# Kernel tuning notes

Measured on AMD Instinct MI355X. Metric: run time of the kernel, lower is better.

Reference implementation:

```python
import jax, jax.numpy as jnp
import numpy as np

N_NODES = 100000  # total nodes (60k type-a + 40k type-b)
N_EDGES = 3200000


def spmm(rows, cols, vals, x):
    # y[r] = sum_e vals[e] * x[cols[e]] for edges with rows[e] == r  (COO SpMM)
    return jax.ops.segment_sum(vals[:, None] * x[cols], rows, num_segments=N_NODES)


def setup_inputs() -> dict:
    key = jax.random.key(0)
    ks = jax.random.split(key, 12)
    d_a, d_b, n_hid, n_out = 256, 128, 256, 64
    s = lambda d: (1.0 / np.sqrt(d)).astype(np.float32)
    return {
        "x_a": jax.random.normal(ks[0], (60000, d_a), dtype=jnp.float32),
        "x_b": jax.random.normal(ks[1], (40000, d_b), dtype=jnp.float32),
        "rows": jax.random.randint(ks[2], (N_EDGES,), 0, N_NODES, dtype=jnp.int32),
        "cols": jax.random.randint(ks[3], (N_EDGES,), 0, N_NODES, dtype=jnp.int32),
        "vals": jax.random.uniform(ks[4], (N_EDGES,), dtype=jnp.float32),
        "W1a": jax.random.normal(ks[5], (d_a, n_hid), dtype=jnp.float32) * s(d_a),
        "b1a": jnp.zeros((n_hid,), dtype=jnp.float32),
        "W1b": jax.random.normal(ks[6], (d_b, n_hid), dtype=jnp.float32) * s(d_b),
        "b1b": jnp.zeros((n_hid,), dtype=jnp.float32),
        "Wf": jax.random.normal(ks[7], (n_hid, n_hid), dtype=jnp.float32) * s(n_hid),
        "bf": jnp.zeros((n_hid,), dtype=jnp.float32),
        "W2": jax.random.normal(ks[8], (n_hid, n_out), dtype=jnp.float32) * s(n_hid),
        "b2": jnp.zeros((n_out,), dtype=jnp.float32),
    }


def reference(x_a, x_b, rows, cols, vals, W1a, b1a, W1b, b1b, Wf, bf, W2, b2):
    # per-type Linear + ReLU (dropout p=0 -> identity in eval/reference)
    h_a = jax.nn.relu(x_a @ W1a + b1a)  # [60000, n_hid]
    h_b = jax.nn.relu(x_b @ W1b + b1b)  # [40000, n_hid]
    x = jnp.concatenate([h_a, h_b], axis=0)  # [N_NODES, n_hid]
    # hop - 1 = 1 intermediate hop: Linear -> SpMM -> ReLU
    x = x @ Wf + bf
    x = spmm(rows, cols, vals, x)
    x = jax.nn.relu(x)
    # output projection then final SpMM aggregation
    x = x @ W2 + b2
    x = spmm(rows, cols, vals, x)  # [N_NODES, n_out]
    return x
```

## Files before the change

kernel.cpp:

```cpp
#include <hip/hip_runtime.h>

#define NN 100000
#define NE 3200000
#define NA 60000
#define NB 40000
#define NHID 256
#define NOUT 64

#define RPB 64
#define NBUCK 1563
#define PBLK 256
#define CHUNK 12500

#define WT_BLKS 704
#define G1_BLKS 938
#define G2_BLKS 626
#define G3_BLKS 1564

typedef unsigned short u16;
typedef unsigned int u32;
typedef __attribute__((ext_vector_type(8))) short short8;
typedef __attribute__((ext_vector_type(4))) float f32x4;

__device__ __forceinline__ float bf2f(u16 u) {
  return __uint_as_float(((u32)u) << 16);
}
__device__ __forceinline__ u16 f2bf(float f) {
  u32 u = __float_as_uint(f);
  u32 r = (u + 0x7fffu + ((u >> 16) & 1u)) >> 16;
  return (u16)r;
}
__device__ __forceinline__ float i8f(u32 dw, int b) {
  return (float)((int)(dw << (24 - 8 * b)) >> 24);
}

__device__ __forceinline__ void gload_lds16(const void* gsrc, void* ldst) {
  __builtin_amdgcn_global_load_lds(
      (const __attribute__((address_space(1))) void*)gsrc,
      (__attribute__((address_space(3))) void*)ldst, 16, 0, 0);
}

template <int BN, int RELU_OUT, int QUANT>
__device__ __forceinline__ void gemm_body(
    int bx, int by, const u16* __restrict__ A, const u16* __restrict__ Bt,
    const float* __restrict__ bias, void* __restrict__ Cout,
    float* __restrict__ scales, int M, int N, int K, u16* As, u16* Bs) {
  constexpr int FI = (BN == 128) ? 4 : 2;
  constexpr int WROWS = FI * 16;

  const int tid = threadIdx.x;
  const int w = tid >> 6;
  const int lane = tid & 63;
  const int bm = bx * 128;
  const int bn = by * BN;
  const int wr = (BN == 128) ? (w >> 1) : w;
  const int wc = (BN == 128) ? (w & 1) : 0;

  f32x4 acc[FI][4];
#pragma unroll
  for (int i = 0; i < FI; ++i)
#pragma unroll
    for (int j = 0; j < 4; ++j) acc[i][j] = (f32x4)0.f;

  for (int k0 = 0; k0 < K; k0 += 32) {
#pragma unroll
    for (int s = 0; s < 2; ++s) {
      const int inst = w * 2 + s;
      const int row = inst * 16 + (lane >> 2);
      int rg = bm + row;
      if (rg > M - 1) rg = M - 1;
      const int c = (lane & 3) ^ ((row >> 1) & 3);
      gload_lds16(A + (size_t)rg * K + k0 + c * 8, &As[inst * 512]);
    }
    if (BN == 128) {
#pragma unroll
      for (int s = 0; s < 2; ++s) {
        const int inst = w * 2 + s;
        const int row = inst * 16 + (lane >> 2);
        const int c = (lane & 3) ^ ((row >> 1) & 3);
        gload_lds16(Bt + (size_t)(bn + row) * K + k0 + c * 8,
                    &Bs[inst * 512]);
      }
    } else {
      const int inst = w;
      const int row = inst * 16 + (lane >> 2);
      const int c = (lane & 3) ^ ((row >> 1) & 3);
      gload_lds16(Bt + (size_t)(bn + row) * K + k0 + c * 8, &Bs[inst * 512]);
    }
    __syncthreads();

    const int kc = lane >> 4;
    short8 af[FI], bfr[4];
#pragma unroll
    for (int i = 0; i < FI; ++i) {
      const int row = wr * WROWS + i * 16 + (lane & 15);
      const int ch = kc ^ ((row >> 1) & 3);
      af[i] = *reinterpret_cast<const short8*>(&As[row * 32 + ch * 8]);
    }
#pragma unroll
    for (int j = 0; j < 4; ++j) {
      const int row = wc * 64 + j * 16 + (lane & 15);
      const int ch = kc ^ ((row >> 1) & 3);
      bfr[j] = *reinterpret_cast<const short8*>(&Bs[row * 32 + ch * 8]);
    }
#pragma unroll
    for (int i = 0; i < FI; ++i)
#pragma unroll
      for (int j = 0; j < 4; ++j)
        acc[i][j] = __builtin_amdgcn_mfma_f32_16x16x32_bf16(af[i], bfr[j],
                                                            acc[i][j], 0, 0, 0);
    __syncthreads();
  }

  if constexpr (QUANT == 1) {
    float bv[4];
#pragma unroll
    for (int j = 0; j < 4; ++j)
      bv[j] = bias[bn + wc * 64 + j * 16 + (lane & 15)];
    const int g = (bn >> 6) + wc;
    u32* zq = (u32*)Cout;
#pragma unroll
    for (int i = 0; i < FI; ++i) {
#pragma unroll
      for (int r = 0; r < 4; ++r) {
        float o[4];
#pragma unroll
        for (int j = 0; j < 4; ++j) o[j] = acc[i][j][r] + bv[j];
        float am = fmaxf(fmaxf(fabsf(o[0]), fabsf(o[1])),
                         fmaxf(fabsf(o[2]), fabsf(o[3])));
#pragma unroll
        for (int mk = 1; mk < 16; mk <<= 1) am = fmaxf(am, __shfl_xor(am, mk));
        const float sinv = am > 0.f ? 127.f / am : 0.f;
        const float scv = am > 0.f ? am / 127.f : 0.f;
        const int q0 = __float2int_rn(o[0] * sinv);
        const int q1 = __float2int_rn(o[1] * sinv);
        const int q2 = __float2int_rn(o[2] * sinv);
        const int q3 = __float2int_rn(o[3] * sinv);
        const u32 dw = (q0 & 0xff) | ((q1 & 0xff) << 8) | ((q2 & 0xff) << 16) |
                       ((q3 & 0xff) << 24);
        const int row = bm + wr * WROWS + i * 16 + (lane >> 4) * 4 + r;
        if (row < M) {
          zq[(size_t)row * 64 + g * 16 + (lane & 15)] = dw;
          if ((lane & 15) == 0) scales[(size_t)row * 4 + g] = scv;
        }
      }
    }
  } else if constexpr (QUANT == 2) {
    float bv[4];
#pragma unroll
    for (int j = 0; j < 4; ++j) bv[j] = bias[j * 16 + (lane & 15)];
    u32* zq = (u32*)Cout;
#pragma unroll
    for (int i = 0; i < FI; ++i) {
#pragma unroll
      for (int r = 0; r < 4; ++r) {
        float o[4];
#pragma unroll
        for (int j = 0; j < 4; ++j) o[j] = acc[i][j][r] + bv[j];
        float am = fmaxf(fmaxf(fabsf(o[0]), fabsf(o[1])),
                         fmaxf(fabsf(o[2]), fabsf(o[3])));
#pragma unroll
        for (int mk = 1; mk < 16; mk <<= 1) am = fmaxf(am, __shfl_xor(am, mk));
        const float sinv = am > 0.f ? 127.f / am : 0.f;
        const float scv = am > 0.f ? am / 127.f : 0.f;
        const int q0 = __float2int_rn(o[0] * sinv);
        const int q1 = __float2int_rn(o[1] * sinv);
        const int q2 = __float2int_rn(o[2] * sinv);
        const int q3 = __float2int_rn(o[3] * sinv);
        const u32 dw = (q0 & 0xff) | ((q1 & 0xff) << 8) | ((q2 & 0xff) << 16) |
                       ((q3 & 0xff) << 24);
        const int row = bm + wr * WROWS + i * 16 + (lane >> 4) * 4 + r;
        if (row < M) {
          zq[(size_t)row * 16 + (lane & 15)] = dw;
          if ((lane & 15) == 0) scales[row] = scv;
        }
      }
    }
  } else {
    u16* C = (u16*)Cout;
#pragma unroll
    for (int i = 0; i < FI; ++i) {
#pragma unroll
      for (int j = 0; j < 4; ++j) {
        const int col = bn + wc * 64 + j * 16 + (lane & 15);
        const float bv = bias[col];
#pragma unroll
        for (int r = 0; r < 4; ++r) {
          const int row = bm + wr * WROWS + i * 16 + (lane >> 4) * 4 + r;
          if (row < M) {
            float o = acc[i][j][r] + bv;
            if (RELU_OUT) o = fmaxf(o, 0.f);
            C[(size_t)row * N + col] = f2bf(o);
          }
        }
      }
    }
  }
}

__device__ __forceinline__ void gemm_af32(
    int bx, int by, const float* __restrict__ Af, const u16* __restrict__ Bt,
    const float* __restrict__ bias, u16* __restrict__ C, int M, int K,
    u16* As, u16* Bs) {
  constexpr int N = 256;
  const int tid = threadIdx.x;
  const int w = tid >> 6;
  const int lane = tid & 63;
  const int bm = bx * 128;
  const int bn = by * 128;
  const int wr = w >> 1;
  const int wc = w & 1;

  f32x4 acc[4][4];
#pragma unroll
  for (int i = 0; i < 4; ++i)
#pragma unroll
    for (int j = 0; j < 4; ++j) acc[i][j] = (f32x4)0.f;

  const int arow = tid >> 1;
  const int ahalf = tid & 1;
  int arg = bm + arow;
  if (arg > M - 1) arg = M - 1;
  const int asw = (arow >> 1) & 3;

  for (int k0 = 0; k0 < K; k0 += 32) {
#pragma unroll
    for (int s = 0; s < 2; ++s) {
      const int inst = w * 2 + s;
      const int row = inst * 16 + (lane >> 2);
      const int c = (lane & 3) ^ ((row >> 1) & 3);
      gload_lds16(Bt + (size_t)(bn + row) * K + k0 + c * 8, &Bs[inst * 512]);
    }
    {
      const float4* src = reinterpret_cast<const float4*>(
          Af + (size_t)arg * K + k0 + ahalf * 16);
      const float4 v0 = src[0], v1 = src[1], v2 = src[2], v3 = src[3];
      short8 lo, hi;
      lo[0] = (short)f2bf(v0.x); lo[1] = (short)f2bf(v0.y);
      lo[2] = (short)f2bf(v0.z); lo[3] = (short)f2bf(v0.w);
      lo[4] = (short)f2bf(v1.x); lo[5] = (short)f2bf(v1.y);
      lo[6] = (short)f2bf(v1.z); lo[7] = (short)f2bf(v1.w);
      hi[0] = (short)f2bf(v2.x); hi[1] = (short)f2bf(v2.y);
      hi[2] = (short)f2bf(v2.z); hi[3] = (short)f2bf(v2.w);
      hi[4] = (short)f2bf(v3.x); hi[5] = (short)f2bf(v3.y);
      hi[6] = (short)f2bf(v3.z); hi[7] = (short)f2bf(v3.w);
      short8* dst = reinterpret_cast<short8*>(As + arow * 32);
      dst[(ahalf * 2) ^ asw] = lo;
      dst[(ahalf * 2 + 1) ^ asw] = hi;
    }
    __syncthreads();

    const int kc = lane >> 4;
    short8 af[4], bfr[4];
#pragma unroll
    for (int i = 0; i < 4; ++i) {
      const int row = wr * 64 + i * 16 + (lane & 15);
      const int ch = kc ^ ((row >> 1) & 3);
      af[i] = *reinterpret_cast<const short8*>(&As[row * 32 + ch * 8]);
    }
#pragma unroll
    for (int j = 0; j < 4; ++j) {
      const int row = wc * 64 + j * 16 + (lane & 15);
      const int ch = kc ^ ((row >> 1) & 3);
      bfr[j] = *reinterpret_cast<const short8*>(&Bs[row * 32 + ch * 8]);
    }
#pragma unroll
    for (int i = 0; i < 4; ++i)
#pragma unroll
      for (int j = 0; j < 4; ++j)
        acc[i][j] = __builtin_amdgcn_mfma_f32_16x16x32_bf16(af[i], bfr[j],
                                                            acc[i][j], 0, 0, 0);
    __syncthreads();
  }

#pragma unroll
  for (int i = 0; i < 4; ++i) {
#pragma unroll
    for (int j = 0; j < 4; ++j) {
      const int col = bn + wc * 64 + j * 16 + (lane & 15);
      const float bv = bias[col];
#pragma unroll
      for (int r = 0; r < 4; ++r) {
        const int row = bm + wr * 64 + i * 16 + (lane >> 4) * 4 + r;
        if (row < M) {
          float o = fmaxf(acc[i][j][r] + bv, 0.f);
          C[(size_t)row * N + col] = f2bf(o);
        }
      }
    }
  }
}

template <int BN, int RELU_OUT, int QUANT>
__global__ __launch_bounds__(256) void gemm_mfma(
    const u16* __restrict__ A, const u16* __restrict__ Bt,
    const float* __restrict__ bias, void* __restrict__ Cout,
    float* __restrict__ scales, int M, int N, int K) {
  __shared__ __align__(16) u16 As[128 * 32];
  __shared__ __align__(16) u16 Bs[BN * 32];
  gemm_body<BN, RELU_OUT, QUANT>(blockIdx.x, blockIdx.y, A, Bt, bias, Cout,
                                 scales, M, N, K, As, Bs);
}

__global__ __launch_bounds__(256) void prep(
    const float* __restrict__ W1a, const float* __restrict__ W1b,
    const float* __restrict__ Wf, const float* __restrict__ W2,
    u16* __restrict__ W1at, u16* __restrict__ W1bt, u16* __restrict__ Wft,
    u16* __restrict__ W2t, const int* __restrict__ rows,
    int* __restrict__ cnt) {
  __shared__ int hsh[NBUCK];
  const int b = blockIdx.x;
  const int tid = threadIdx.x;
  if (b < WT_BLKS) {
    const int i = b * 256 + tid;
    if (i < 65536) {
      const int n = i >> 8, k = i & 255;
      W1at[i] = f2bf(W1a[k * 256 + n]);
    } else if (i < 98304) {
      const int t = i - 65536;
      const int n = t >> 7, k = t & 127;
      W1bt[t] = f2bf(W1b[k * 256 + n]);
    } else if (i < 163840) {
      const int t = i - 98304;
      const int n = t >> 8, k = t & 255;
      Wft[t] = f2bf(Wf[k * 256 + n]);
    } else if (i < 180224) {
      const int t = i - 163840;
      const int n = t >> 8, p = t & 255;
      const int f = ((p >> 6) << 6) + ((p & 3) << 4) + ((p >> 2) & 15);
      W2t[t] = f2bf(W2[f * 64 + n]);
    }
  } else {
    const int blk = b - WT_BLKS;
    for (int i = tid; i < NBUCK; i += 256) hsh[i] = 0;
    __syncthreads();
    const int s = blk * CHUNK;
    const int e = s + CHUNK;
    for (int i = s + tid; i < e; i += 256) atomicAdd(&hsh[rows[i] >> 6], 1);
    __syncthreads();
    for (int i = tid; i < NBUCK; i += 256) cnt[i * PBLK + blk] = hsh[i];
  }
}

__global__ __launch_bounds__(256) void gemm12_s1(
    const float* __restrict__ xa, const u16* __restrict__ W1at,
    const float* __restrict__ b1a, const float* __restrict__ xb,
    const u16* __restrict__ W1bt, const float* __restrict__ b1b,
    u16* __restrict__ h, int* __restrict__ cnt, int* __restrict__ btot) {
  __shared__ __align__(16) u16 As[128 * 32];
  __shared__ __align__(16) u16 Bs[128 * 32];
  const int b = blockIdx.x;
  if (b < G1_BLKS) {
    gemm_af32(b % 469, b / 469, xa, W1at, b1a, h, NA, 256, As, Bs);
  } else if (b < G1_BLKS + G2_BLKS) {
    const int t = b - G1_BLKS;
    gemm_af32(t % 313, t / 313, xb, W1bt, b1b, h + (size_t)NA * NHID, NB, 128,
              As, Bs);
  } else {
    int* lds = (int*)As;
    const int bu = b - (G1_BLKS + G2_BLKS);
    const int t = threadIdx.x;
    const int v = cnt[bu * PBLK + t];
    lds[t] = v;
    __syncthreads();
#pragma unroll
    for (int off = 1; off < 256; off <<= 1) {
      const int x = (t >= off) ? lds[t - off] : 0;
      __syncthreads();
      lds[t] += x;
      __syncthreads();
    }
    cnt[bu * PBLK + t] = lds[t] - v;
    if (t == 255) btot[bu] = lds[255];
  }
}

__global__ __launch_bounds__(256) void gemm3_s2_p3(
    const u16* __restrict__ h, const u16* __restrict__ Wft,
    const float* __restrict__ bfv, u32* __restrict__ zq,
    float* __restrict__ zscale, const int* __restrict__ btot,
    int* __restrict__ bstart, const int* __restrict__ rows,
    const int* __restrict__ cols, const float* __restrict__ vals,
    const int* __restrict__ cnt, int2* __restrict__ edges) {
  __shared__ __align__(16) u16 As[128 * 32];
  __shared__ __align__(16) u16 Bs[128 * 32];
  const int b = blockIdx.x;
  const int t = threadIdx.x;
  if (b < G3_BLKS) {
    gemm_body<128, 0, 1>(b % 782, b / 782, h, Wft, bfv, zq, zscale, NN, NHID,
                         256, As, Bs);
  } else if (b == G3_BLKS) {
    int* lds = (int*)As;
    int carry = 0;
    for (int base = 0; base < NBUCK; base += 256) {
      const int i = base + t;
      const int v = (i < NBUCK) ? btot[i] : 0;
      lds[t] = v;
      __syncthreads();
#pragma unroll
      for (int off = 1; off < 256; off <<= 1) {
        const int x = (t >= off) ? lds[t - off] : 0;
        __syncthreads();
        lds[t] += x;
        __syncthreads();
      }
      const int excl = lds[t] - v;
      const int tot = lds[255];
      if (i < NBUCK) bstart[i] = carry + excl;
      __syncthreads();
      carry += tot;
    }
    if (t == 0) bstart[NBUCK] = NE;
  } else {
    const int blk = b - (G3_BLKS + 1);
    int* lbs = (int*)As;
    int* tmp = (int*)Bs;
    int carry = 0;
    for (int base = 0; base < NBUCK; base += 256) {
      const int i = base + t;
      const int v = (i < NBUCK) ? btot[i] : 0;
      tmp[t] = v;
      __syncthreads();
#pragma unroll
      for (int off = 1; off < 256; off <<= 1) {
        const int x = (t >= off) ? tmp[t - off] : 0;
        __syncthreads();
        tmp[t] += x;
        __syncthreads();
      }
      if (i < NBUCK) lbs[i] = carry + tmp[t] - v;
      const int tot = tmp[255];
      __syncthreads();
      carry += tot;
    }
    for (int bu = t; bu < NBUCK; bu += 256) lbs[bu] += cnt[bu * PBLK + blk];
    __syncthreads();
    const int s = blk * CHUNK;
    const int e = s + CHUNK;
    for (int i = s + t; i < e; i += 256) {
      const int r = rows[i];
      const int pos = atomicAdd(&lbs[r >> 6], 1);
      edges[pos] = make_int2(cols[i] | ((r & 63) << 17), __float_as_int(vals[i]));
    }
  }
}

__global__ __launch_bounds__(256) void sort_bucket(
    const int* __restrict__ bstart, const int2* __restrict__ edges,
    int2* __restrict__ edges2, int* __restrict__ rptr) {
  __shared__ int hist[RPB];
  __shared__ int sc[RPB];
  __shared__ int cur[RPB];
  const int bu = blockIdx.x;
  const int t = threadIdx.x;
  const int s = bstart[bu], e = bstart[bu + 1];
  if (t < RPB) hist[t] = 0;
  __syncthreads();
  for (int i = s + t; i < e; i += 256)
    atomicAdd(&hist[(edges[i].x >> 17) & 63], 1);
  __syncthreads();
  const int hv = (t < RPB) ? hist[t] : 0;
  if (t < RPB) sc[t] = hv;
  __syncthreads();
#pragma unroll
  for (int off = 1; off < RPB; off <<= 1) {
    const int x = (t >= off && t < RPB) ? sc[t - off] : 0;
    __syncthreads();
    if (t < RPB) sc[t] += x;
    __syncthreads();
  }
  if (t < RPB) {
    const int base = s + sc[t] - hv;
    cur[t] = base;
    const int grow = bu * RPB + t;
    if (grow < NN) rptr[grow] = base;
  }
  if (bu == 0 && t == 0) rptr[NN] = NE;
  __syncthreads();
  for (int i = s + t; i < e; i += 256) {
    const int2 ed = edges[i];
    const int lr = (ed.x >> 17) & 63;
    const int pos = atomicAdd(&cur[lr], 1);
    edges2[pos] = make_int2(ed.x & 0x1FFFF, ed.y);
  }
}

__global__ __launch_bounds__(256) void spmm256_q8(
    const int* __restrict__ ptr, const int2* __restrict__ edges,
    const u32* __restrict__ Zq, const float* __restrict__ scales,
    u16* __restrict__ Yb) {
  const int wid = (int)((blockIdx.x * (size_t)256 + threadIdx.x) >> 6);
  const int lane = threadIdx.x & 63;
  if (wid >= NN) return;
  const int s = ptr[wid], e = ptr[wid + 1];
  const int gsel = lane >> 4;
  float a0 = 0.f, a1 = 0.f, a2 = 0.f, a3 = 0.f;
  int j = s;
  for (; j + 7 < e; j += 8) {
    int2 ed[8];
#pragma unroll
    for (int q = 0; q < 8; ++q) ed[q] = edges[j + q];
    u32 dw[8];
    float sc[8];
#pragma unroll
    for (int q = 0; q < 8; ++q) {
      dw[q] = Zq[(size_t)ed[q].x * 64 + lane];
      sc[q] = scales[(size_t)ed[q].x * 4 + gsel];
    }
#pragma unroll
    for (int q = 0; q < 8; ++q) {
      const float vs = __int_as_float(ed[q].y) * sc[q];
      a0 += vs * i8f(dw[q], 0);
      a1 += vs * i8f(dw[q], 1);
      a2 += vs * i8f(dw[q], 2);
      a3 += vs * i8f(dw[q], 3);
    }
  }
  for (; j < e; ++j) {
    const int2 e0 = edges[j];
    const u32 dw = Zq[(size_t)e0.x * 64 + lane];
    const float vs =
        __int_as_float(e0.y) * scales[(size_t)e0.x * 4 + gsel];
    a0 += vs * i8f(dw, 0);
    a1 += vs * i8f(dw, 1);
    a2 += vs * i8f(dw, 2);
    a3 += vs * i8f(dw, 3);
  }
  ushort4 o;
  o.x = f2bf(fmaxf(a0, 0.f));
  o.y = f2bf(fmaxf(a1, 0.f));
  o.z = f2bf(fmaxf(a2, 0.f));
  o.w = f2bf(fmaxf(a3, 0.f));
  reinterpret_cast<ushort4*>(Yb + (size_t)wid * 256)[lane] = o;
}

__global__ __launch_bounds__(256) void spmm64_q8(
    const int* __restrict__ ptr, const int2* __restrict__ edges,
    const u32* __restrict__ Z2q, const float* __restrict__ zsc2,
    float* __restrict__ Y) {
  const int wid = (int)((blockIdx.x * (size_t)256 + threadIdx.x) >> 6);
  const int lane = threadIdx.x & 63;
  if (wid >= NN) return;
  const int s = ptr[wid], e = ptr[wid + 1];
  const int dwi = lane & 15;
  const int byi = lane >> 4;
  float acc = 0.f;
  int j = s;
  for (; j + 7 < e; j += 8) {
    int2 ed[8];
#pragma unroll
    for (int q = 0; q < 8; ++q) ed[q] = edges[j + q];
    u32 dw[8];
    float sc[8];
#pragma unroll
    for (int q = 0; q < 8; ++q) {
      dw[q] = Z2q[(size_t)ed[q].x * 16 + dwi];
      sc[q] = zsc2[ed[q].x];
    }
#pragma unroll
    for (int q = 0; q < 8; ++q)
      acc += __int_as_float(ed[q].y) * sc[q] * i8f(dw[q], byi);
  }
  for (; j < e; ++j) {
    const int2 e0 = edges[j];
    const u32 dw = Z2q[(size_t)e0.x * 16 + dwi];
    acc += __int_as_float(e0.y) * zsc2[e0.x] * i8f(dw, byi);
  }
  Y[(size_t)wid * 64 + lane] = acc;
}

extern "C" void kernel_launch(void* const* d_in, const int* in_sizes, int n_in,
                              void* d_out, int out_size, void* d_ws,
                              size_t ws_size, hipStream_t stream) {
  const float* x_a  = (const float*)d_in[0];
  const float* x_b  = (const float*)d_in[1];
  const int*   rows = (const int*)d_in[2];
  const int*   cols = (const int*)d_in[3];
  const float* vals = (const float*)d_in[4];
  const float* W1a  = (const float*)d_in[5];
  const float* b1a  = (const float*)d_in[6];
  const float* W1b  = (const float*)d_in[7];
  const float* b1b  = (const float*)d_in[8];
  const float* Wf   = (const float*)d_in[9];
  const float* bf   = (const float*)d_in[10];
  const float* W2   = (const float*)d_in[11];
  const float* b2   = (const float*)d_in[12];
  float* out = (float*)d_out;

  char* p = (char*)d_ws;
  u16* h    = (u16*)p;  p += (size_t)NN * NHID * 2;
  u32* zq   = (u32*)p;  p += (size_t)NN * 64 * 4;
  float* zscale = (float*)p; p += (size_t)NN * 4 * 4;
  u32* z2q  = (u32*)p;  p += (size_t)NN * 16 * 4;
  float* zsc2 = (float*)p; p += (size_t)NN * 4;
  int2* edges2 = (int2*)p; p += (size_t)NE * 8;
  u16* W1at = (u16*)p;  p += 256 * 256 * 2;
  u16* W1bt = (u16*)p;  p += 256 * 128 * 2;
  u16* Wft  = (u16*)p;  p += 256 * 256 * 2;
  u16* W2t  = (u16*)p;  p += 64 * 256 * 2;
  int2* edges = (int2*)p; p += (size_t)NE * 8;
  int* cnt    = (int*)p;  p += (size_t)NBUCK * PBLK * 4;
  int* btot   = (int*)p;  p += (size_t)((NBUCK + 3) & ~3) * 4;
  int* bstart = (int*)p;  p += (size_t)((NBUCK + 4) & ~3) * 4;
  int* rptr   = (int*)p;  p += (size_t)(NN + 4) * 4;
  u16* s1b = h;

  prep<<<WT_BLKS + PBLK, 256, 0, stream>>>(W1a, W1b, Wf, W2, W1at, W1bt, Wft,
                                           W2t, rows, cnt);

  gemm12_s1<<<G1_BLKS + G2_BLKS + NBUCK, 256, 0, stream>>>(
      x_a, W1at, b1a, x_b, W1bt, b1b, h, cnt, btot);

  gemm3_s2_p3<<<G3_BLKS + 1 + PBLK, 256, 0, stream>>>(
      h, Wft, bf, zq, zscale, btot, bstart, rows, cols, vals, cnt, edges);

  sort_bucket<<<NBUCK, 256, 0, stream>>>(bstart, edges, edges2, rptr);

  spmm256_q8<<<(NN * 64 + 255) / 256, 256, 0, stream>>>(rptr, edges2, zq,
                                                        zscale, s1b);
  gemm_mfma<64, 0, 2><<<dim3((NN + 127) / 128, 1), 256, 0, stream>>>(
      s1b, W2t, b2, z2q, zsc2, NN, NOUT, 256);
  spmm64_q8<<<(NN * 64 + 255) / 256, 256, 0, stream>>>(rptr, edges2, z2q,
                                                       zsc2, out);
}
```

Baseline: 479.4 us.

## Pack sorted edges into 32-bit words and widen GEMM blocks to full N

Sorted CSR edges are packed into one 32-bit word each, holding a 17-bit column index and the edge value as fp16 in the upper 15 bits (sign bit dropped, which is fine because the values are non-negative). This halves the edge traffic in both SpMM passes. The first-layer and Wf GEMMs now run with 512-thread blocks that each cover all 256 output columns, so the A tile is loaded once instead of twice and the block count halves. The cost is reduced precision on the edge values and larger per-block LDS, and the scan kernels are adapted to the new block size.

```diff
diff --git a/kernel.cpp b/kernel.cpp
--- a/kernel.cpp
+++ b/kernel.cpp
@@ -13,9 +13,9 @@
 #define CHUNK 12500
 
 #define WT_BLKS 704
-#define G1_BLKS 938
-#define G2_BLKS 626
-#define G3_BLKS 1564
+#define G1_BLKS 469
+#define G2_BLKS 313
+#define G3_BLKS 782
 
 typedef unsigned short u16;
 typedef unsigned int u32;
@@ -33,6 +33,18 @@
 __device__ __forceinline__ float i8f(u32 dw, int b) {
   return (float)((int)(dw << (24 - 8 * b)) >> 24);
 }
+__device__ __forceinline__ u16 f2h(float f) {
+  _Float16 h = (_Float16)f;
+  u16 r;
+  __builtin_memcpy(&r, &h, 2);
+  return r;
+}
+__device__ __forceinline__ float h2f(u32 b15) {
+  u16 hb = (u16)b15;
+  _Float16 h;
+  __builtin_memcpy(&h, &hb, 2);
+  return (float)h;
+}
 
 __device__ __forceinline__ void gload_lds16(const void* gsrc, void* ldst) {
   __builtin_amdgcn_global_load_lds(
@@ -40,60 +52,46 @@
       (__attribute__((address_space(3))) void*)ldst, 16, 0, 0);
 }
 
-template <int BN, int RELU_OUT, int QUANT>
-__device__ __forceinline__ void gemm_body(
-    int bx, int by, const u16* __restrict__ A, const u16* __restrict__ Bt,
+template <int QUANT>
+__device__ __forceinline__ void gemm8_body(
+    int bx, const u16* __restrict__ A, const u16* __restrict__ Bt,
     const float* __restrict__ bias, void* __restrict__ Cout,
-    float* __restrict__ scales, int M, int N, int K, u16* As, u16* Bs) {
-  constexpr int FI = (BN == 128) ? 4 : 2;
-  constexpr int WROWS = FI * 16;
-
+    float* __restrict__ scales, int M, int K, u16* As, u16* Bs) {
   const int tid = threadIdx.x;
   const int w = tid >> 6;
   const int lane = tid & 63;
   const int bm = bx * 128;
-  const int bn = by * BN;
-  const int wr = (BN == 128) ? (w >> 1) : w;
-  const int wc = (BN == 128) ? (w & 1) : 0;
-
-  f32x4 acc[FI][4];
-#pragma unroll
-  for (int i = 0; i < FI; ++i)
+  const int wr = w >> 2;
+  const int wc = w & 3;
+
+  f32x4 acc[4][4];
+#pragma unroll
+  for (int i = 0; i < 4; ++i)
 #pragma unroll
     for (int j = 0; j < 4; ++j) acc[i][j] = (f32x4)0.f;
 
   for (int k0 = 0; k0 < K; k0 += 32) {
+    {
+      const int row = w * 16 + (lane >> 2);
+      int rg = bm + row;
+      if (rg > M - 1) rg = M - 1;
+      const int c = (lane & 3) ^ ((row >> 1) & 3);
+      gload_lds16(A + (size_t)rg * K + k0 + c * 8, &As[w * 512]);
+    }
 #pragma unroll
     for (int s = 0; s < 2; ++s) {
       const int inst = w * 2 + s;
       const int row = inst * 16 + (lane >> 2);
-      int rg = bm + row;
-      if (rg > M - 1) rg = M - 1;
       const int c = (lane & 3) ^ ((row >> 1) & 3);
-      gload_lds16(A + (size_t)rg * K + k0 + c * 8, &As[inst * 512]);
-    }
-    if (BN == 128) {
-#pragma unroll
-      for (int s = 0; s < 2; ++s) {
-        const int inst = w * 2 + s;
-        const int row = inst * 16 + (lane >> 2);
-        const int c = (lane & 3) ^ ((row >> 1) & 3);
-        gload_lds16(Bt + (size_t)(bn + row) * K + k0 + c * 8,
-                    &Bs[inst * 512]);
-      }
-    } else {
-      const int inst = w;
-      const int row = inst * 16 + (lane >> 2);
-      const int c = (lane & 3) ^ ((row >> 1) & 3);
-      gload_lds16(Bt + (size_t)(bn + row) * K + k0 + c * 8, &Bs[inst * 512]);
+      gload_lds16(Bt + (size_t)row * K + k0 + c * 8, &Bs[inst * 512]);
     }
     __syncthreads();
 
     const int kc = lane >> 4;
-    short8 af[FI], bfr[4];
-#pragma unroll
-    for (int i = 0; i < FI; ++i) {
-      const int row = wr * WROWS + i * 16 + (lane & 15);
+    short8 af[4], bfr[4];
+#pragma unroll
+    for (int i = 0; i < 4; ++i) {
+      const int row = wr * 64 + i * 16 + (lane & 15);
       const int ch = kc ^ ((row >> 1) & 3);
       af[i] = *reinterpret_cast<const short8*>(&As[row * 32 + ch * 8]);
     }
@@ -104,7 +102,7 @@
       bfr[j] = *reinterpret_cast<const short8*>(&Bs[row * 32 + ch * 8]);
     }
 #pragma unroll
-    for (int i = 0; i < FI; ++i)
+    for (int i = 0; i < 4; ++i)
 #pragma unroll
       for (int j = 0; j < 4; ++j)
         acc[i][j] = __builtin_amdgcn_mfma_f32_16x16x32_bf16(af[i], bfr[j],
@@ -115,12 +113,11 @@
   if constexpr (QUANT == 1) {
     float bv[4];
 #pragma unroll
-    for (int j = 0; j < 4; ++j)
-      bv[j] = bias[bn + wc * 64 + j * 16 + (lane & 15)];
-    const int g = (bn >> 6) + wc;
+    for (int j = 0; j < 4; ++j) bv[j] = bias[wc * 64 + j * 16 + (lane & 15)];
+    const int g = wc;
     u32* zq = (u32*)Cout;
 #pragma unroll
-    for (int i = 0; i < FI; ++i) {
+    for (int i = 0; i < 4; ++i) {
 #pragma unroll
       for (int r = 0; r < 4; ++r) {
         float o[4];
@@ -138,59 +135,27 @@
         const int q3 = __float2int_rn(o[3] * sinv);
         const u32 dw = (q0 & 0xff) | ((q1 & 0xff) << 8) | ((q2 & 0xff) << 16) |
                        ((q3 & 0xff) << 24);
-        const int row = bm + wr * WROWS + i * 16 + (lane >> 4) * 4 + r;
+        const int row = bm + wr * 64 + i * 16 + (lane >> 4) * 4 + r;
         if (row < M) {
           zq[(size_t)row * 64 + g * 16 + (lane & 15)] = dw;
           if ((lane & 15) == 0) scales[(size_t)row * 4 + g] = scv;
         }
       }
     }
-  } else if constexpr (QUANT == 2) {
-    float bv[4];
-#pragma unroll
-    for (int j = 0; j < 4; ++j) bv[j] = bias[j * 16 + (lane & 15)];
-    u32* zq = (u32*)Cout;
-#pragma unroll
-    for (int i = 0; i < FI; ++i) {
-#pragma unroll
-      for (int r = 0; r < 4; ++r) {
-        float o[4];
-#pragma unroll
-        for (int j = 0; j < 4; ++j) o[j] = acc[i][j][r] + bv[j];
-        float am = fmaxf(fmaxf(fabsf(o[0]), fabsf(o[1])),
-                         fmaxf(fabsf(o[2]), fabsf(o[3])));
-#pragma unroll
-        for (int mk = 1; mk < 16; mk <<= 1) am = fmaxf(am, __shfl_xor(am, mk));
-        const float sinv = am > 0.f ? 127.f / am : 0.f;
-        const float scv = am > 0.f ? am / 127.f : 0.f;
-        const int q0 = __float2int_rn(o[0] * sinv);
-        const int q1 = __float2int_rn(o[1] * sinv);
-        const int q2 = __float2int_rn(o[2] * sinv);
-        const int q3 = __float2int_rn(o[3] * sinv);
-        const u32 dw = (q0 & 0xff) | ((q1 & 0xff) << 8) | ((q2 & 0xff) << 16) |
-                       ((q3 & 0xff) << 24);
-        const int row = bm + wr * WROWS + i * 16 + (lane >> 4) * 4 + r;
-        if (row < M) {
-          zq[(size_t)row * 16 + (lane & 15)] = dw;
-          if ((lane & 15) == 0) scales[row] = scv;
-        }
-      }
-    }
   } else {
     u16* C = (u16*)Cout;
 #pragma unroll
-    for (int i = 0; i < FI; ++i) {
+    for (int i = 0; i < 4; ++i) {
 #pragma unroll
       for (int j = 0; j < 4; ++j) {
-        const int col = bn + wc * 64 + j * 16 + (lane & 15);
+        const int col = wc * 64 + j * 16 + (lane & 15);
         const float bv = bias[col];
 #pragma unroll
         for (int r = 0; r < 4; ++r) {
-          const int row = bm + wr * WROWS + i * 16 + (lane >> 4) * 4 + r;
+          const int row = bm + wr * 64 + i * 16 + (lane >> 4) * 4 + r;
           if (row < M) {
-            float o = acc[i][j][r] + bv;
-            if (RELU_OUT) o = fmaxf(o, 0.f);
-            C[(size_t)row * N + col] = f2bf(o);
+            float o = fmaxf(acc[i][j][r] + bv, 0.f);
+            C[(size_t)row * 256 + col] = f2bf(o);
           }
         }
       }
@@ -198,18 +163,16 @@
   }
 }
 
-__device__ __forceinline__ void gemm_af32(
-    int bx, int by, const float* __restrict__ Af, const u16* __restrict__ Bt,
+__device__ __forceinline__ void gemm8_af32(
+    int bx, const float* __restrict__ Af, const u16* __restrict__ Bt,
     const float* __restrict__ bias, u16* __restrict__ C, int M, int K,
     u16* As, u16* Bs) {
-  constexpr int N = 256;
   const int tid = threadIdx.x;
   const int w = tid >> 6;
   const int lane = tid & 63;
   const int bm = bx * 128;
-  const int bn = by * 128;
-  const int wr = w >> 1;
-  const int wc = w & 1;
+  const int wr = w >> 2;
+  const int wc = w & 3;
 
   f32x4 acc[4][4];
 #pragma unroll
@@ -217,8 +180,8 @@
 #pragma unroll
     for (int j = 0; j < 4; ++j) acc[i][j] = (f32x4)0.f;
 
-  const int arow = tid >> 1;
-  const int ahalf = tid & 1;
+  const int arow = tid >> 2;
+  const int aq = tid & 3;
   int arg = bm + arow;
   if (arg > M - 1) arg = M - 1;
   const int asw = (arow >> 1) & 3;
@@ -229,24 +192,18 @@
       const int inst = w * 2 + s;
       const int row = inst * 16 + (lane >> 2);
       const int c = (lane & 3) ^ ((row >> 1) & 3);
-      gload_lds16(Bt + (size_t)(bn + row) * K + k0 + c * 8, &Bs[inst * 512]);
+      gload_lds16(Bt + (size_t)row * K + k0 + c * 8, &Bs[inst * 512]);
     }
     {
-      const float4* src = reinterpret_cast<const float4*>(
-          Af + (size_t)arg * K + k0 + ahalf * 16);
-      const float4 v0 = src[0], v1 = src[1], v2 = src[2], v3 = src[3];
-      short8 lo, hi;
-      lo[0] = (short)f2bf(v0.x); lo[1] = (short)f2bf(v0.y);
-      lo[2] = (short)f2bf(v0.z); lo[3] = (short)f2bf(v0.w);
-      lo[4] = (short)f2bf(v1.x); lo[5] = (short)f2bf(v1.y);
-      lo[6] = (short)f2bf(v1.z); lo[7] = (short)f2bf(v1.w);
-      hi[0] = (short)f2bf(v2.x); hi[1] = (short)f2bf(v2.y);
-      hi[2] = (short)f2bf(v2.z); hi[3] = (short)f2bf(v2.w);
-      hi[4] = (short)f2bf(v3.x); hi[5] = (short)f2bf(v3.y);
-      hi[6] = (short)f2bf(v3.z); hi[7] = (short)f2bf(v3.w);
-      short8* dst = reinterpret_cast<short8*>(As + arow * 32);
-      dst[(ahalf * 2) ^ asw] = lo;
-      dst[(ahalf * 2 + 1) ^ asw] = hi;
+      const float4* src =
+          reinterpret_cast<const float4*>(Af + (size_t)arg * K + k0 + aq * 8);
+      const float4 v0 = src[0], v1 = src[1];
+      short8 ch;
+      ch[0] = (short)f2bf(v0.x); ch[1] = (short)f2bf(v0.y);
+      ch[2] = (short)f2bf(v0.z); ch[3] = (short)f2bf(v0.w);
+      ch[4] = (short)f2bf(v1.x); ch[5] = (short)f2bf(v1.y);
+      ch[6] = (short)f2bf(v1.z); ch[7] = (short)f2bf(v1.w);
+      reinterpret_cast<short8*>(As + arow * 32)[aq ^ asw] = ch;
     }
     __syncthreads();
 
@@ -277,29 +234,106 @@
   for (int i = 0; i < 4; ++i) {
 #pragma unroll
     for (int j = 0; j < 4; ++j) {
-      const int col = bn + wc * 64 + j * 16 + (lane & 15);
+      const int col = wc * 64 + j * 16 + (lane & 15);
       const float bv = bias[col];
 #pragma unroll
       for (int r = 0; r < 4; ++r) {
         const int row = bm + wr * 64 + i * 16 + (lane >> 4) * 4 + r;
         if (row < M) {
           float o = fmaxf(acc[i][j][r] + bv, 0.f);
-          C[(size_t)row * N + col] = f2bf(o);
+          C[(size_t)row * 256 + col] = f2bf(o);
         }
       }
     }
   }
 }
 
-template <int BN, int RELU_OUT, int QUANT>
-__global__ __launch_bounds__(256) void gemm_mfma(
+__global__ __launch_bounds__(256) void gemm4_q8(
     const u16* __restrict__ A, const u16* __restrict__ Bt,
-    const float* __restrict__ bias, void* __restrict__ Cout,
-    float* __restrict__ scales, int M, int N, int K) {
+    const float* __restrict__ bias, u32* __restrict__ zq,
+    float* __restrict__ scales, int M, int K) {
   __shared__ __align__(16) u16 As[128 * 32];
-  __shared__ __align__(16) u16 Bs[BN * 32];
-  gemm_body<BN, RELU_OUT, QUANT>(blockIdx.x, blockIdx.y, A, Bt, bias, Cout,
-                                 scales, M, N, K, As, Bs);
+  __shared__ __align__(16) u16 Bs[64 * 32];
+  const int tid = threadIdx.x;
+  const int w = tid >> 6;
+  const int lane = tid & 63;
+  const int bm = blockIdx.x * 128;
+
+  f32x4 acc[2][4];
+#pragma unroll
+  for (int i = 0; i < 2; ++i)
+#pragma unroll
+    for (int j = 0; j < 4; ++j) acc[i][j] = (f32x4)0.f;
+
+  for (int k0 = 0; k0 < K; k0 += 32) {
+#pragma unroll
+    for (int s = 0; s < 2; ++s) {
+      const int inst = w * 2 + s;
+      const int row = inst * 16 + (lane >> 2);
+      int rg = bm + row;
+      if (rg > M - 1) rg = M - 1;
+      const int c = (lane & 3) ^ ((row >> 1) & 3);
+      gload_lds16(A + (size_t)rg * K + k0 + c * 8, &As[inst * 512]);
+    }
+    {
+      const int row = w * 16 + (lane >> 2);
+      const int c = (lane & 3) ^ ((row >> 1) & 3);
+      gload_lds16(Bt + (size_t)row * K + k0 + c * 8, &Bs[w * 512]);
+    }
+    __syncthreads();
+
+    const int kc = lane >> 4;
+    short8 af[2], bfr[4];
+#pragma unroll
+    for (int i = 0; i < 2; ++i) {
+      const int row = w * 32 + i * 16 + (lane & 15);
+      const int ch = kc ^ ((row >> 1) & 3);
+      af[i] = *reinterpret_cast<const short8*>(&As[row * 32 + ch * 8]);
+    }
+#pragma unroll
+    for (int j = 0; j < 4; ++j) {
+      const int row = j * 16 + (lane & 15);
+      const int ch = kc ^ ((row >> 1) & 3);
+      bfr[j] = *reinterpret_cast<const short8*>(&Bs[row * 32 + ch * 8]);
+    }
+#pragma unroll
+    for (int i = 0; i < 2; ++i)
+#pragma unroll
+      for (int j = 0; j < 4; ++j)
+        acc[i][j] = __builtin_amdgcn_mfma_f32_16x16x32_bf16(af[i], bfr[j],
+                                                            acc[i][j], 0, 0, 0);
+    __syncthreads();
+  }
+
+  float bv[4];
+#pragma unroll
+  for (int j = 0; j < 4; ++j) bv[j] = bias[j * 16 + (lane & 15)];
+#pragma unroll
+  for (int i = 0; i < 2; ++i) {
+#pragma unroll
+    for (int r = 0; r < 4; ++r) {
+      float o[4];
+#pragma unroll
+      for (int j = 0; j < 4; ++j) o[j] = acc[i][j][r] + bv[j];
+      float am = fmaxf(fmaxf(fabsf(o[0]), fabsf(o[1])),
+                       fmaxf(fabsf(o[2]), fabsf(o[3])));
+#pragma unroll
+      for (int mk = 1; mk < 16; mk <<= 1) am = fmaxf(am, __shfl_xor(am, mk));
+      const float sinv = am > 0.f ? 127.f / am : 0.f;
+      const float scv = am > 0.f ? am / 127.f : 0.f;
+      const int q0 = __float2int_rn(o[0] * sinv);
+      const int q1 = __float2int_rn(o[1] * sinv);
+      const int q2 = __float2int_rn(o[2] * sinv);
+      const int q3 = __float2int_rn(o[3] * sinv);
+      const u32 dw = (q0 & 0xff) | ((q1 & 0xff) << 8) | ((q2 & 0xff) << 16) |
+                     ((q3 & 0xff) << 24);
+      const int row = bm + w * 32 + i * 16 + (lane >> 4) * 4 + r;
+      if (row < M) {
+        zq[(size_t)row * 16 + (lane & 15)] = dw;
+        if ((lane & 15) == 0) scales[row] = scv;
+      }
+    }
+  }
 }
 
 __global__ __launch_bounds__(256) void prep(
@@ -342,40 +376,39 @@
   }
 }
 
-__global__ __launch_bounds__(256) void gemm12_s1(
+__global__ __launch_bounds__(512) void gemm12_s1(
     const float* __restrict__ xa, const u16* __restrict__ W1at,
     const float* __restrict__ b1a, const float* __restrict__ xb,
     const u16* __restrict__ W1bt, const float* __restrict__ b1b,
     u16* __restrict__ h, int* __restrict__ cnt, int* __restrict__ btot) {
   __shared__ __align__(16) u16 As[128 * 32];
-  __shared__ __align__(16) u16 Bs[128 * 32];
+  __shared__ __align__(16) u16 Bs[256 * 32];
   const int b = blockIdx.x;
   if (b < G1_BLKS) {
-    gemm_af32(b % 469, b / 469, xa, W1at, b1a, h, NA, 256, As, Bs);
+    gemm8_af32(b, xa, W1at, b1a, h, NA, 256, As, Bs);
   } else if (b < G1_BLKS + G2_BLKS) {
-    const int t = b - G1_BLKS;
-    gemm_af32(t % 313, t / 313, xb, W1bt, b1b, h + (size_t)NA * NHID, NB, 128,
-              As, Bs);
+    gemm8_af32(b - G1_BLKS, xb, W1bt, b1b, h + (size_t)NA * NHID, NB, 128, As,
+               Bs);
   } else {
     int* lds = (int*)As;
     const int bu = b - (G1_BLKS + G2_BLKS);
     const int t = threadIdx.x;
-    const int v = cnt[bu * PBLK + t];
+    const int v = (t < PBLK) ? cnt[bu * PBLK + t] : 0;
     lds[t] = v;
     __syncthreads();
 #pragma unroll
-    for (int off = 1; off < 256; off <<= 1) {
+    for (int off = 1; off < PBLK; off <<= 1) {
       const int x = (t >= off) ? lds[t - off] : 0;
       __syncthreads();
       lds[t] += x;
       __syncthreads();
     }
-    cnt[bu * PBLK + t] = lds[t] - v;
-    if (t == 255) btot[bu] = lds[255];
-  }
-}
-
-__global__ __launch_bounds__(256) void gemm3_s2_p3(
+    if (t < PBLK) cnt[bu * PBLK + t] = lds[t] - v;
+    if (t == PBLK - 1) btot[bu] = lds[t];
+  }
+}
+
+__global__ __launch_bounds__(512) void gemm3_s2_p3(
     const u16* __restrict__ h, const u16* __restrict__ Wft,
     const float* __restrict__ bfv, u32* __restrict__ zq,
     float* __restrict__ zscale, const int* __restrict__ btot,
@@ -383,29 +416,28 @@
     const int* __restrict__ cols, const float* __restrict__ vals,
     const int* __restrict__ cnt, int2* __restrict__ edges) {
   __shared__ __align__(16) u16 As[128 * 32];
-  __shared__ __align__(16) u16 Bs[128 * 32];
+  __shared__ __align__(16) u16 Bs[256 * 32];
   const int b = blockIdx.x;
   const int t = threadIdx.x;
   if (b < G3_BLKS) {
-    gemm_body<128, 0, 1>(b % 782, b / 782, h, Wft, bfv, zq, zscale, NN, NHID,
-                         256, As, Bs);
+    gemm8_body<1>(b, h, Wft, bfv, zq, zscale, NN, 256, As, Bs);
   } else if (b == G3_BLKS) {
     int* lds = (int*)As;
     int carry = 0;
-    for (int base = 0; base < NBUCK; base += 256) {
+    for (int base = 0; base < NBUCK; base += 512) {
       const int i = base + t;
       const int v = (i < NBUCK) ? btot[i] : 0;
       lds[t] = v;
       __syncthreads();
 #pragma unroll
-      for (int off = 1; off < 256; off <<= 1) {
+      for (int off = 1; off < 512; off <<= 1) {
         const int x = (t >= off) ? lds[t - off] : 0;
         __syncthreads();
         lds[t] += x;
         __syncthreads();
       }
       const int excl = lds[t] - v;
-      const int tot = lds[255];
+      const int tot = lds[511];
       if (i < NBUCK) bstart[i] = carry + excl;
       __syncthreads();
       carry += tot;
@@ -416,38 +448,39 @@
     int* lbs = (int*)As;
     int* tmp = (int*)Bs;
     int carry = 0;
-    for (int base = 0; base < NBUCK; base += 256) {
+    for (int base = 0; base < NBUCK; base += 512) {
       const int i = base + t;
       const int v = (i < NBUCK) ? btot[i] : 0;
       tmp[t] = v;
       __syncthreads();
 #pragma unroll
-      for (int off = 1; off < 256; off <<= 1) {
+      for (int off = 1; off < 512; off <<= 1) {
         const int x = (t >= off) ? tmp[t - off] : 0;
         __syncthreads();
         tmp[t] += x;
         __syncthreads();
       }
       if (i < NBUCK) lbs[i] = carry + tmp[t] - v;
-      const int tot = tmp[255];
+      const int tot = tmp[511];
       __syncthreads();
       carry += tot;
     }
-    for (int bu = t; bu < NBUCK; bu += 256) lbs[bu] += cnt[bu * PBLK + blk];
+    for (int bu = t; bu < NBUCK; bu += 512) lbs[bu] += cnt[bu * PBLK + blk];
     __syncthreads();
     const int s = blk * CHUNK;
     const int e = s + CHUNK;
-    for (int i = s + t; i < e; i += 256) {
+    for (int i = s + t; i < e; i += 512) {
       const int r = rows[i];
       const int pos = atomicAdd(&lbs[r >> 6], 1);
-      edges[pos] = make_int2(cols[i] | ((r & 63) << 17), __float_as_int(vals[i]));
+      edges[pos] =
+          make_int2(cols[i] | ((r & 63) << 17), __float_as_int(vals[i]));
     }
   }
 }
 
 __global__ __launch_bounds__(256) void sort_bucket(
     const int* __restrict__ bstart, const int2* __restrict__ edges,
-    int2* __restrict__ edges2, int* __restrict__ rptr) {
+    u32* __restrict__ edges2, int* __restrict__ rptr) {
   __shared__ int hist[RPB];
   __shared__ int sc[RPB];
   __shared__ int cur[RPB];
@@ -481,12 +514,13 @@
     const int2 ed = edges[i];
     const int lr = (ed.x >> 17) & 63;
     const int pos = atomicAdd(&cur[lr], 1);
-    edges2[pos] = make_int2(ed.x & 0x1FFFF, ed.y);
+    edges2[pos] = (u32)(ed.x & 0x1FFFF) |
+                  ((u32)f2h(__int_as_float(ed.y)) << 17);
   }
 }
 
 __global__ __launch_bounds__(256) void spmm256_q8(
-    const int* __restrict__ ptr, const int2* __restrict__ edges,
+    const int* __restrict__ ptr, const u32* __restrict__ edges,
     const u32* __restrict__ Zq, const float* __restrict__ scales,
     u16* __restrict__ Yb) {
   const int wid = (int)((blockIdx.x * (size_t)256 + threadIdx.x) >> 6);
@@ -497,19 +531,20 @@
   float a0 = 0.f, a1 = 0.f, a2 = 0.f, a3 = 0.f;
   int j = s;
   for (; j + 7 < e; j += 8) {
-    int2 ed[8];
+    u32 ed[8];
 #pragma unroll
     for (int q = 0; q < 8; ++q) ed[q] = edges[j + q];
     u32 dw[8];
     float sc[8];
 #pragma unroll
     for (int q = 0; q < 8; ++q) {
-      dw[q] = Zq[(size_t)ed[q].x * 64 + lane];
-      sc[q] = scales[(size_t)ed[q].x * 4 + gsel];
+      const int c = ed[q] & 0x1FFFF;
+      dw[q] = Zq[(size_t)c * 64 + lane];
+      sc[q] = scales[(size_t)c * 4 + gsel];
     }
 #pragma unroll
     for (int q = 0; q < 8; ++q) {
-      const float vs = __int_as_float(ed[q].y) * sc[q];
+      const float vs = h2f(ed[q] >> 17) * sc[q];
       a0 += vs * i8f(dw[q], 0);
       a1 += vs * i8f(dw[q], 1);
       a2 += vs * i8f(dw[q], 2);
@@ -517,10 +552,10 @@
     }
   }
   for (; j < e; ++j) {
-    const int2 e0 = edges[j];
-    const u32 dw = Zq[(size_t)e0.x * 64 + lane];
-    const float vs =
-        __int_as_float(e0.y) * scales[(size_t)e0.x * 4 + gsel];
+    const u32 ed = edges[j];
+    const int c = ed & 0x1FFFF;
+    const u32 dw = Zq[(size_t)c * 64 + lane];
+    const float vs = h2f(ed >> 17) * scales[(size_t)c * 4 + gsel];
     a0 += vs * i8f(dw, 0);
     a1 += vs * i8f(dw, 1);
     a2 += vs * i8f(dw, 2);
@@ -535,7 +570,7 @@
 }
 
 __global__ __launch_bounds__(256) void spmm64_q8(
-    const int* __restrict__ ptr, const int2* __restrict__ edges,
+    const int* __restrict__ ptr, const u32* __restrict__ edges,
     const u32* __restrict__ Z2q, const float* __restrict__ zsc2,
     float* __restrict__ Y) {
   const int wid = (int)((blockIdx.x * (size_t)256 + threadIdx.x) >> 6);
@@ -547,24 +582,25 @@
   float acc = 0.f;
   int j = s;
   for (; j + 7 < e; j += 8) {
-    int2 ed[8];
+    u32 ed[8];
 #pragma unroll
     for (int q = 0; q < 8; ++q) ed[q] = edges[j + q];
     u32 dw[8];
     float sc[8];
 #pragma unroll
     for (int q = 0; q < 8; ++q) {
-      dw[q] = Z2q[(size_t)ed[q].x * 16 + dwi];
-      sc[q] = zsc2[ed[q].x];
+      const int c = ed[q] & 0x1FFFF;
+      dw[q] = Z2q[(size_t)c * 16 + dwi];
+      sc[q] = zsc2[c];
     }
 #pragma unroll
     for (int q = 0; q < 8; ++q)
-      acc += __int_as_float(ed[q].y) * sc[q] * i8f(dw[q], byi);
+      acc += h2f(ed[q] >> 17) * sc[q] * i8f(dw[q], byi);
   }
   for (; j < e; ++j) {
-    const int2 e0 = edges[j];
-    const u32 dw = Z2q[(size_t)e0.x * 16 + dwi];
-    acc += __int_as_float(e0.y) * zsc2[e0.x] * i8f(dw, byi);
+    const u32 ed = edges[j];
+    const int c = ed & 0x1FFFF;
+    acc += h2f(ed >> 17) * zsc2[c] * i8f(Z2q[(size_t)c * 16 + dwi], byi);
   }
   Y[(size_t)wid * 64 + lane] = acc;
 }
@@ -593,7 +629,7 @@
   float* zscale = (float*)p; p += (size_t)NN * 4 * 4;
   u32* z2q  = (u32*)p;  p += (size_t)NN * 16 * 4;
   float* zsc2 = (float*)p; p += (size_t)NN * 4;
-  int2* edges2 = (int2*)p; p += (size_t)NE * 8;
+  u32* edges2 = (u32*)p;  p += (size_t)NE * 4;
   u16* W1at = (u16*)p;  p += 256 * 256 * 2;
   u16* W1bt = (u16*)p;  p += 256 * 128 * 2;
   u16* Wft  = (u16*)p;  p += 256 * 256 * 2;
@@ -608,18 +644,17 @@
   prep<<<WT_BLKS + PBLK, 256, 0, stream>>>(W1a, W1b, Wf, W2, W1at, W1bt, Wft,
                                            W2t, rows, cnt);
 
-  gemm12_s1<<<G1_BLKS + G2_BLKS + NBUCK, 256, 0, stream>>>(
+  gemm12_s1<<<G1_BLKS + G2_BLKS + NBUCK, 512, 0, stream>>>(
       x_a, W1at, b1a, x_b, W1bt, b1b, h, cnt, btot);
 
-  gemm3_s2_p3<<<G3_BLKS + 1 + PBLK, 256, 0, stream>>>(
+  gemm3_s2_p3<<<G3_BLKS + 1 + PBLK, 512, 0, stream>>>(
       h, Wft, bf, zq, zscale, btot, bstart, rows, cols, vals, cnt, edges);
 
   sort_bucket<<<NBUCK, 256, 0, stream>>>(bstart, edges, edges2, rptr);
 
   spmm256_q8<<<(NN * 64 + 255) / 256, 256, 0, stream>>>(rptr, edges2, zq,
                                                         zscale, s1b);
-  gemm_mfma<64, 0, 2><<<dim3((NN + 127) / 128, 1), 256, 0, stream>>>(
-      s1b, W2t, b2, z2q, zsc2, NN, NOUT, 256);
+  gemm4_q8<<<G3_BLKS, 256, 0, stream>>>(s1b, W2t, b2, z2q, zsc2, NN, 256);
   spmm64_q8<<<(NN * 64 + 255) / 256, 256, 0, stream>>>(rptr, edges2, z2q,
                                                        zsc2, out);
 }
```

After: 423.0 us. 11.8% less time.
